# Optimization experiments

Measured on AMD Instinct MI355X. Metric: run time of the kernel, lower is better.

The kernel has to match this reference:

```python
import jax, jax.numpy as jnp
import numpy as np

TOP_K = 2
EPS = 1e-10


def setup_inputs() -> dict:
    key = jax.random.key(0)
    k1, k2 = jax.random.split(key)
    B, S, D, E = 4, 4096, 4096, 64
    hidden_states = jax.random.normal(k1, (B, S, D), dtype=jnp.float32)
    # router weight, scaled like a standard linear init
    w_router = jax.random.normal(k2, (D, E), dtype=jnp.float32) / np.sqrt(D)
    return {"hidden_states": hidden_states, "w_router": w_router}


def reference(hidden_states, w_router):
    # router: [B,S,D] x [D,E] -> [B,S,E]
    router_logits = jnp.einsum("bsd,de->bse", hidden_states, w_router)
    # balanced_assignment: softmax, global load, penalty, adjusted top-k
    routing_probs = jax.nn.softmax(router_logits, axis=-1)
    current_load = routing_probs.sum(axis=(0, 1))            # [E]
    load_penalty = current_load / (current_load.mean() + EPS)  # [E]
    adjusted_logits = router_logits - jnp.log(load_penalty + EPS)
    _, expert_indices = jax.lax.top_k(adjusted_logits, TOP_K)  # [B,S,top_k]
    return adjusted_logits, expert_indices
```

## Files before the change

### kernel.cpp

```cpp
#include <hip/hip_runtime.h>
#include <math.h>

#define ROWS 16384
#define DD   4096
#define EE   64
#define EPSF 1e-10f

#define BM     64
#define KSPLIT 2
#define KRANGE (DD / KSPLIT)
#define KT     64
#define NPH    (KRANGE / KT)
#define WTILE  8192
#define BTILE  (2 * WTILE)

typedef __attribute__((ext_vector_type(8))) short short8;
typedef __attribute__((ext_vector_type(4))) float f32x4;
typedef __attribute__((ext_vector_type(4))) unsigned u32x4;

__device__ __forceinline__ void split2x8(const float f[8], u32x4& w0,
                                         u32x4& w1) {
#pragma unroll
  for (int i = 0; i < 4; ++i) {
    float fa = f[2 * i], fb = f[2 * i + 1];
    unsigned ua = __float_as_uint(fa), ub = __float_as_uint(fb);
    unsigned ra = ua + 0x7fffu + ((ua >> 16) & 1u);
    unsigned rb = ub + 0x7fffu + ((ub >> 16) & 1u);
    w0[i] = (rb & 0xffff0000u) | (ra >> 16);
    fa -= __uint_as_float(ra & 0xffff0000u);
    fb -= __uint_as_float(rb & 0xffff0000u);
    ua = __float_as_uint(fa); ub = __float_as_uint(fb);
    ra = ua + 0x7fffu + ((ua >> 16) & 1u);
    rb = ub + 0x7fffu + ((ub >> 16) & 1u);
    w1[i] = (rb & 0xffff0000u) | (ra >> 16);
  }
}

__device__ __forceinline__ void dma16(const void* g, void* l) {
  __builtin_amdgcn_global_load_lds(
      (const __attribute__((address_space(1))) unsigned int*)g,
      (__attribute__((address_space(3))) unsigned int*)l, 16, 0, 0);
}

__global__ __launch_bounds__(256) void k_wsplit(const float* __restrict__ wr,
                                                unsigned char* __restrict__ out,
                                                float* __restrict__ logits,
                                                float* __restrict__ g_load) {
  const int kt = blockIdx.x;
  const int t = threadIdx.x;
  const int lane = t & 63, wv = t >> 6;
  if (blockIdx.x == 0 && t < 64) g_load[t] = 0.f;
  {
    float4 z = {0.f, 0.f, 0.f, 0.f};
    float4* lp4 = (float4*)logits + (size_t)blockIdx.x * 2048 + t;
#pragma unroll
    for (int i = 0; i < 8; ++i) lp4[i * 256] = z;
  }
  float f[8];
  const float* wp = wr + (size_t)(kt * 32 + wv * 8) * EE + lane;
#pragma unroll
  for (int j = 0; j < 8; ++j) f[j] = wp[(size_t)j * EE];
  u32x4 w0, w1;
  split2x8(f, w0, w1);
  const int et = lane >> 4;
  const int lp = wv * 16 + (lane & 15);
  unsigned char* base = out + (size_t)kt * WTILE + et * 1024 + lp * 16;
  *(u32x4*)(base + 0 * 4096) = w0;
  *(u32x4*)(base + 1 * 4096) = w1;
}

__global__ __launch_bounds__(256) void k_gemm(
    const float* __restrict__ h, const unsigned char* __restrict__ wsp,
    float* __restrict__ logits) {
  __shared__ alignas(16) unsigned char smem[2 * BTILE];

  const int t = threadIdx.x;
  const int lane = t & 63;
  const int wv = t >> 6;
  const int row0 = (blockIdx.x >> 1) * BM;
  const int ks = blockIdx.x & 1;

  f32x4 acc[4] = {};

  const float* ap = h + (size_t)(row0 + wv * 16 + (lane & 15)) * DD +
                    ks * KRANGE + (lane >> 4) * 8;
  const unsigned char* wbase = wsp + (size_t)ks * NPH * BTILE;
  const int dmaoff = t * 16;

  float4 c0, c1, c2, c3, n0, n1, n2, n3;

#pragma unroll
  for (int i = 0; i < 4; ++i)
    dma16(wbase + i * 4096 + dmaoff, smem + i * 4096 + dmaoff);
  c0 = *(const float4*)(ap);
  c1 = *(const float4*)(ap + 4);
  c2 = *(const float4*)(ap + 32);
  c3 = *(const float4*)(ap + 36);

  for (int kt = 0; kt < NPH; ++kt) {
    const int buf = kt & 1;
    asm volatile("s_waitcnt vmcnt(0)" ::: "memory");
    __syncthreads();

    if (kt + 1 < NPH) {
      const unsigned char* ws = wbase + (size_t)(kt + 1) * BTILE;
      unsigned char* nb = smem + (buf ^ 1) * BTILE;
#pragma unroll
      for (int i = 0; i < 4; ++i)
        dma16(ws + i * 4096 + dmaoff, nb + i * 4096 + dmaoff);
      const float* p = ap + (size_t)(kt + 1) * KT;
      n0 = *(const float4*)(p);
      n1 = *(const float4*)(p + 4);
      n2 = *(const float4*)(p + 32);
      n3 = *(const float4*)(p + 36);
    }

    const unsigned char* lb = smem + buf * BTILE;
#pragma unroll
    for (int sub = 0; sub < 2; ++sub) {
      const unsigned char* sb = lb + sub * WTILE;
      short8 bf[2][4];
#pragma unroll
      for (int p = 0; p < 2; ++p)
#pragma unroll
        for (int e = 0; e < 4; ++e)
          bf[p][e] = *(const short8*)&sb[p * 4096 + e * 1024 + lane * 16];

      const float4 a0 = sub ? c2 : c0;
      const float4 a1 = sub ? c3 : c1;
      const float af[8] = {a0.x, a0.y, a0.z, a0.w, a1.x, a1.y, a1.z, a1.w};
      u32x4 q0, q1;
      split2x8(af, q0, q1);
      const short8 ah0 = __builtin_bit_cast(short8, q0);
      const short8 ah1 = __builtin_bit_cast(short8, q1);
#pragma unroll
      for (int e = 0; e < 4; ++e) {
        f32x4 c = acc[e];
        c = __builtin_amdgcn_mfma_f32_16x16x32_bf16(ah0, bf[0][e], c, 0, 0, 0);
        c = __builtin_amdgcn_mfma_f32_16x16x32_bf16(ah0, bf[1][e], c, 0, 0, 0);
        c = __builtin_amdgcn_mfma_f32_16x16x32_bf16(ah1, bf[0][e], c, 0, 0, 0);
        acc[e] = c;
      }
    }

    if (kt + 1 < NPH) { c0 = n0; c1 = n1; c2 = n2; c3 = n3; }
  }

  const int rbase = row0 + wv * 16 + (lane >> 4) * 4;
  const int col = lane & 15;
#pragma unroll
  for (int e = 0; e < 4; ++e)
#pragma unroll
    for (int r = 0; r < 4; ++r)
      atomicAdd(&logits[(size_t)(rbase + r) * EE + e * 16 + col],
                acc[e][r]);
}

__global__ __launch_bounds__(256) void k_softload(
    const float* __restrict__ logits, float* __restrict__ g_load) {
  __shared__ float red[4][64];
  const int lane = threadIdx.x & 63;
  const int wv = threadIdx.x >> 6;
  float accp = 0.f;
#pragma unroll 4
  for (int i = 0; i < 16; ++i) {
    int row = blockIdx.x * 64 + wv * 16 + i;
    float x = logits[(size_t)row * EE + lane];
    float m = x;
#pragma unroll
    for (int off = 32; off > 0; off >>= 1) m = fmaxf(m, __shfl_xor(m, off, 64));
    float p = __expf(x - m);
    float s = p;
#pragma unroll
    for (int off = 32; off > 0; off >>= 1) s += __shfl_xor(s, off, 64);
    accp += p / s;
  }
  red[wv][lane] = accp;
  __syncthreads();
  if (wv == 0) {
    float s = red[0][lane] + red[1][lane] + red[2][lane] + red[3][lane];
    atomicAdd(&g_load[lane], s);
  }
}

__global__ __launch_bounds__(256) void k_top2(float* __restrict__ logits,
                                              const float* __restrict__ g_load,
                                              float* __restrict__ idx_out) {
  int t = threadIdx.x;
  int lane = t & 63;
  int wv = t >> 6;
  int row = blockIdx.x * 4 + wv;

  float v0 = g_load[lane];
  float s0 = v0;
#pragma unroll
  for (int off = 32; off > 0; off >>= 1) s0 += __shfl_xor(s0, off, 64);
  float lp = logf(v0 / (s0 * (1.f / 64.f) + EPSF) + EPSF);

  size_t base = (size_t)row * EE;
  float a = logits[base + lane] - lp;
  logits[base + lane] = a;

  float v = a;
  int idx = lane;
#pragma unroll
  for (int off = 32; off > 0; off >>= 1) {
    float ov = __shfl_xor(v, off, 64);
    int oi = __shfl_xor(idx, off, 64);
    if (ov > v || (ov == v && oi < idx)) { v = ov; idx = oi; }
  }
  int i1 = idx;

  float a2 = (lane == i1) ? -INFINITY : a;
  v = a2;
  idx = lane;
#pragma unroll
  for (int off = 32; off > 0; off >>= 1) {
    float ov = __shfl_xor(v, off, 64);
    int oi = __shfl_xor(idx, off, 64);
    if (ov > v || (ov == v && oi < idx)) { v = ov; idx = oi; }
  }
  int i2 = idx;

  if (lane == 0) {
    idx_out[(size_t)row * 2 + 0] = (float)i1;
    idx_out[(size_t)row * 2 + 1] = (float)i2;
  }
}

extern "C" void kernel_launch(void* const* d_in, const int* in_sizes, int n_in,
                              void* d_out, int out_size, void* d_ws,
                              size_t ws_size, hipStream_t stream) {
  const float* h = (const float*)d_in[0];
  const float* wr = (const float*)d_in[1];
  float* out = (float*)d_out;
  float* logits = out;
  float* idx_out = out + (size_t)ROWS * EE;
  float* g_load = (float*)d_ws;
  unsigned char* wsp = (unsigned char*)d_ws + 512;

  k_wsplit<<<DD / 32, 256, 0, stream>>>(wr, wsp, logits, g_load);
  k_gemm<<<(ROWS / BM) * KSPLIT, 256, 0, stream>>>(h, wsp, logits);
  k_softload<<<ROWS / 64, 256, 0, stream>>>(logits, g_load);
  k_top2<<<ROWS / 4, 256, 0, stream>>>(logits, g_load, idx_out);
}
```

Before: 400.0 us.

## Fuse all stages into one cooperative persistent kernel with grid syncs

Replaces the four separate launches with a single cooperative kernel of 512 blocks that runs weight split and zeroing, then the GEMM, then the softmax load reduction, then the adjusted top-2, with grid-wide syncs between phases. Each block keeps its 32 rows of logits in shared memory between the load phase and the top-2 phase, so the second global read of logits is avoided. This removes three kernel launch gaps and one pass over the logits. In exchange it adds grid barrier costs and requires all 512 blocks to be co-resident. If the cooperative launch fails it falls back to the old four-kernel path.

```diff
diff --git a/kernel.cpp b/kernel.cpp
--- a/kernel.cpp
+++ b/kernel.cpp
@@ -1,5 +1,8 @@
 #include <hip/hip_runtime.h>
+#include <hip/hip_cooperative_groups.h>
 #include <math.h>
+
+namespace cg = cooperative_groups;
 
 #define ROWS 16384
 #define DD   4096
@@ -42,20 +45,10 @@
       (__attribute__((address_space(3))) unsigned int*)l, 16, 0, 0);
 }
 
-__global__ __launch_bounds__(256) void k_wsplit(const float* __restrict__ wr,
-                                                unsigned char* __restrict__ out,
-                                                float* __restrict__ logits,
-                                                float* __restrict__ g_load) {
-  const int kt = blockIdx.x;
-  const int t = threadIdx.x;
+__device__ __forceinline__ void wsplit_body(int kt, int t,
+                                            const float* __restrict__ wr,
+                                            unsigned char* __restrict__ out) {
   const int lane = t & 63, wv = t >> 6;
-  if (blockIdx.x == 0 && t < 64) g_load[t] = 0.f;
-  {
-    float4 z = {0.f, 0.f, 0.f, 0.f};
-    float4* lp4 = (float4*)logits + (size_t)blockIdx.x * 2048 + t;
-#pragma unroll
-    for (int i = 0; i < 8; ++i) lp4[i * 256] = z;
-  }
   float f[8];
   const float* wp = wr + (size_t)(kt * 32 + wv * 8) * EE + lane;
 #pragma unroll
@@ -69,16 +62,13 @@
   *(u32x4*)(base + 1 * 4096) = w1;
 }
 
-__global__ __launch_bounds__(256) void k_gemm(
-    const float* __restrict__ h, const unsigned char* __restrict__ wsp,
-    float* __restrict__ logits) {
-  __shared__ alignas(16) unsigned char smem[2 * BTILE];
-
-  const int t = threadIdx.x;
+__device__ __forceinline__ void gemm_body(
+    int b, int t, unsigned char* smem, const float* __restrict__ h,
+    const unsigned char* __restrict__ wsp, float* __restrict__ logits) {
   const int lane = t & 63;
   const int wv = t >> 6;
-  const int row0 = (blockIdx.x >> 1) * BM;
-  const int ks = blockIdx.x & 1;
+  const int row0 = (b >> 1) * BM;
+  const int ks = b & 1;
 
   f32x4 acc[4] = {};
 
@@ -154,6 +144,119 @@
     for (int r = 0; r < 4; ++r)
       atomicAdd(&logits[(size_t)(rbase + r) * EE + e * 16 + col],
                 acc[e][r]);
+}
+
+__global__ __launch_bounds__(256, 2) void k_fused(
+    const float* __restrict__ h, const float* __restrict__ wr,
+    unsigned char* __restrict__ wsp, float* __restrict__ logits,
+    float* __restrict__ g_load, float* __restrict__ idx_out) {
+  __shared__ alignas(16) unsigned char smem[2 * BTILE];
+  cg::grid_group grid = cg::this_grid();
+  const int b = blockIdx.x;
+  const int t = threadIdx.x;
+  const int lane = t & 63;
+  const int wv = t >> 6;
+
+  if (b < 128) {
+    if (b == 0 && t < 64) g_load[t] = 0.f;
+    wsplit_body(b, t, wr, wsp);
+  } else if (b < 256) {
+    float4 z = {0.f, 0.f, 0.f, 0.f};
+    float4* lp4 = (float4*)logits + (size_t)(b - 128) * 2048 + t;
+#pragma unroll
+    for (int i = 0; i < 8; ++i) lp4[i * 256] = z;
+  }
+  grid.sync();
+
+  gemm_body(b, t, smem, h, wsp, logits);
+  grid.sync();
+
+  float* sl2 = (float*)smem;
+  float* red = (float*)(smem + 8192);
+  const int rows0 = b * 32;
+  float accp = 0.f;
+#pragma unroll
+  for (int i = 0; i < 8; ++i) {
+    const int row = rows0 + wv * 8 + i;
+    const float x = logits[(size_t)row * EE + lane];
+    sl2[(wv * 8 + i) * 64 + lane] = x;
+    float m = x;
+#pragma unroll
+    for (int off = 32; off > 0; off >>= 1) m = fmaxf(m, __shfl_xor(m, off, 64));
+    const float p = __expf(x - m);
+    float s = p;
+#pragma unroll
+    for (int off = 32; off > 0; off >>= 1) s += __shfl_xor(s, off, 64);
+    accp += p / s;
+  }
+  red[wv * 64 + lane] = accp;
+  __syncthreads();
+  if (wv == 0) {
+    float s = red[0 * 64 + lane] + red[1 * 64 + lane] + red[2 * 64 + lane] +
+              red[3 * 64 + lane];
+    atomicAdd(&g_load[lane], s);
+  }
+  grid.sync();
+
+  float v0 = g_load[lane];
+  float s0 = v0;
+#pragma unroll
+  for (int off = 32; off > 0; off >>= 1) s0 += __shfl_xor(s0, off, 64);
+  const float lp = logf(v0 / (s0 * (1.f / 64.f) + EPSF) + EPSF);
+
+#pragma unroll
+  for (int i = 0; i < 8; ++i) {
+    const int row = rows0 + wv * 8 + i;
+    const float a = sl2[(wv * 8 + i) * 64 + lane] - lp;
+    logits[(size_t)row * EE + lane] = a;
+
+    float v = a;
+    int idx = lane;
+#pragma unroll
+    for (int off = 32; off > 0; off >>= 1) {
+      float ov = __shfl_xor(v, off, 64);
+      int oi = __shfl_xor(idx, off, 64);
+      if (ov > v || (ov == v && oi < idx)) { v = ov; idx = oi; }
+    }
+    const int i1 = idx;
+    float a2 = (lane == i1) ? -INFINITY : a;
+    v = a2;
+    idx = lane;
+#pragma unroll
+    for (int off = 32; off > 0; off >>= 1) {
+      float ov = __shfl_xor(v, off, 64);
+      int oi = __shfl_xor(idx, off, 64);
+      if (ov > v || (ov == v && oi < idx)) { v = ov; idx = oi; }
+    }
+    const int i2 = idx;
+    if (lane == 0) {
+      idx_out[(size_t)row * 2 + 0] = (float)i1;
+      idx_out[(size_t)row * 2 + 1] = (float)i2;
+    }
+  }
+}
+
+__global__ __launch_bounds__(256) void k_wsplit(const float* __restrict__ wr,
+                                                unsigned char* __restrict__ out,
+                                                float* __restrict__ logits,
+                                                float* __restrict__ g_load) {
+  const int kt = blockIdx.x;
+  const int t = threadIdx.x;
+  if (blockIdx.x == 0 && t < 64) g_load[t] = 0.f;
+  {
+    float4 z = {0.f, 0.f, 0.f, 0.f};
+    float4* lp4 = (float4*)logits + (size_t)blockIdx.x * 2048 + t;
+#pragma unroll
+    for (int i = 0; i < 8; ++i) lp4[i * 256] = z;
+  }
+  wsplit_body(kt, t, wr, out);
+}
+
+__global__ __launch_bounds__(256) void k_gemm(
+    const float* __restrict__ h, const unsigned char* __restrict__ wsp,
+    float* __restrict__ logits) {
+  __shared__ alignas(16) unsigned char smem[2 * BTILE];
+  gemm_body(blockIdx.x, threadIdx.x, smem, h, wsp, logits);
 }
 
 __global__ __launch_bounds__(256) void k_softload(
@@ -239,8 +342,15 @@
   float* g_load = (float*)d_ws;
   unsigned char* wsp = (unsigned char*)d_ws + 512;
 
-  k_wsplit<<<DD / 32, 256, 0, stream>>>(wr, wsp, logits, g_load);
-  k_gemm<<<(ROWS / BM) * KSPLIT, 256, 0, stream>>>(h, wsp, logits);
-  k_softload<<<ROWS / 64, 256, 0, stream>>>(logits, g_load);
-  k_top2<<<ROWS / 4, 256, 0, stream>>>(logits, g_load, idx_out);
-}
+  void* args[6] = {(void*)&h,      (void*)&wr,     (void*)&wsp,
+                   (void*)&logits, (void*)&g_load, (void*)&idx_out};
+  hipError_t err = hipLaunchCooperativeKernel(
+      (const void*)k_fused, dim3((ROWS / BM) * KSPLIT), dim3(256), args, 0,
+      stream);
+  if (err != hipSuccess) {
+    k_wsplit<<<DD / 32, 256, 0, stream>>>(wr, wsp, logits, g_load);
+    k_gemm<<<(ROWS / BM) * KSPLIT, 256, 0, stream>>>(h, wsp, logits);
+    k_softload<<<ROWS / 64, 256, 0, stream>>>(logits, g_load);
+    k_top2<<<ROWS / 4, 256, 0, stream>>>(logits, g_load, idx_out);
+  }
+}
```

Result: slower. 563.4 us (+40.9%).

## Fuse softmax load reduction into GEMM via last-block split-K epilogue

Applied to the files above, without the earlier changes.

The separate softmax/load kernel is removed. Each of the two split-K GEMM blocks atomically adds into a workspace partial buffer and then bumps a per-row-block counter, and the block that arrives second reads the finished logits, writes them to the output and accumulates the softmax load. This saves one kernel launch and one full pass over the logits. In exchange it adds threadfences, a counter atomic, an extra copy from the partial buffer into the output, and an imbalanced tail where only half the blocks run the epilogue.

```diff
diff --git a/kernel.cpp b/kernel.cpp
--- a/kernel.cpp
+++ b/kernel.cpp
@@ -44,17 +44,21 @@
 
 __global__ __launch_bounds__(256) void k_wsplit(const float* __restrict__ wr,
                                                 unsigned char* __restrict__ out,
-                                                float* __restrict__ logits,
-                                                float* __restrict__ g_load) {
+                                                float* __restrict__ partial,
+                                                float* __restrict__ g_load,
+                                                int* __restrict__ counters) {
   const int kt = blockIdx.x;
   const int t = threadIdx.x;
   const int lane = t & 63, wv = t >> 6;
-  if (blockIdx.x == 0 && t < 64) g_load[t] = 0.f;
+  if (blockIdx.x == 0) {
+    if (t < 64) g_load[t] = 0.f;
+    counters[t] = 0;
+  }
   {
     float4 z = {0.f, 0.f, 0.f, 0.f};
-    float4* lp4 = (float4*)logits + (size_t)blockIdx.x * 2048 + t;
-#pragma unroll
-    for (int i = 0; i < 8; ++i) lp4[i * 256] = z;
+    float4* pp = (float4*)partial + (size_t)blockIdx.x * 2048 + t;
+#pragma unroll
+    for (int i = 0; i < 8; ++i) pp[i * 256] = z;
   }
   float f[8];
   const float* wp = wr + (size_t)(kt * 32 + wv * 8) * EE + lane;
@@ -71,14 +75,18 @@
 
 __global__ __launch_bounds__(256) void k_gemm(
     const float* __restrict__ h, const unsigned char* __restrict__ wsp,
-    float* __restrict__ logits) {
+    float* __restrict__ partial, float* __restrict__ logits,
+    float* __restrict__ g_load, int* __restrict__ counters) {
   __shared__ alignas(16) unsigned char smem[2 * BTILE];
+  __shared__ float red[4][64];
+  __shared__ int lastFlag;
 
   const int t = threadIdx.x;
   const int lane = t & 63;
   const int wv = t >> 6;
-  const int row0 = (blockIdx.x >> 1) * BM;
+  const int rb = blockIdx.x >> 1;
   const int ks = blockIdx.x & 1;
+  const int row0 = rb * BM;
 
   f32x4 acc[4] = {};
 
@@ -152,28 +160,29 @@
   for (int e = 0; e < 4; ++e)
 #pragma unroll
     for (int r = 0; r < 4; ++r)
-      atomicAdd(&logits[(size_t)(rbase + r) * EE + e * 16 + col],
+      atomicAdd(&partial[(size_t)(rbase + r) * EE + e * 16 + col],
                 acc[e][r]);
-}
-
-__global__ __launch_bounds__(256) void k_softload(
-    const float* __restrict__ logits, float* __restrict__ g_load) {
-  __shared__ float red[4][64];
-  const int lane = threadIdx.x & 63;
-  const int wv = threadIdx.x >> 6;
+
+  __threadfence();
+  if (t == 0) lastFlag = (atomicAdd(&counters[rb], 1) == 1);
+  __syncthreads();
+  if (!lastFlag) return;
+  __threadfence();
+
   float accp = 0.f;
-#pragma unroll 4
+#pragma unroll
   for (int i = 0; i < 16; ++i) {
-    int row = blockIdx.x * 64 + wv * 16 + i;
-    float x = logits[(size_t)row * EE + lane];
+    const int row = row0 + wv * 16 + i;
+    const float x = partial[(size_t)row * EE + lane];
     float m = x;
 #pragma unroll
     for (int off = 32; off > 0; off >>= 1) m = fmaxf(m, __shfl_xor(m, off, 64));
-    float p = __expf(x - m);
+    const float p = __expf(x - m);
     float s = p;
 #pragma unroll
     for (int off = 32; off > 0; off >>= 1) s += __shfl_xor(s, off, 64);
     accp += p / s;
+    logits[(size_t)row * EE + lane] = x;
   }
   red[wv][lane] = accp;
   __syncthreads();
@@ -236,11 +245,15 @@
   float* out = (float*)d_out;
   float* logits = out;
   float* idx_out = out + (size_t)ROWS * EE;
-  float* g_load = (float*)d_ws;
-  unsigned char* wsp = (unsigned char*)d_ws + 512;
-
-  k_wsplit<<<DD / 32, 256, 0, stream>>>(wr, wsp, logits, g_load);
-  k_gemm<<<(ROWS / BM) * KSPLIT, 256, 0, stream>>>(h, wsp, logits);
-  k_softload<<<ROWS / 64, 256, 0, stream>>>(logits, g_load);
+
+  unsigned char* ws = (unsigned char*)d_ws;
+  float* g_load = (float*)ws;
+  int* counters = (int*)(ws + 256);
+  unsigned char* wsp = ws + 4096;
+  float* partial = (float*)(ws + (2u << 20));
+
+  k_wsplit<<<DD / 32, 256, 0, stream>>>(wr, wsp, partial, g_load, counters);
+  k_gemm<<<(ROWS / BM) * KSPLIT, 256, 0, stream>>>(h, wsp, partial, logits,
+                                                   g_load, counters);
   k_top2<<<ROWS / 4, 256, 0, stream>>>(logits, g_load, idx_out);
 }
```

New measurement: 515.9 us. 1.29x slower.
